# Kernel optimization log

Hardware: AMD Instinct MI355X
Metric: run time of the kernel (lower is better)

The kernel has to match this reference:

```python
import jax, jax.numpy as jnp
import numpy as np

B, N, S, D = 32, 128, 64, 512
MAX_LEN = 5000


def make_pe(d_model, max_len):
    pos = np.arange(max_len, dtype=np.float32)[:, None]
    div = np.exp(np.arange(0, d_model, 2, dtype=np.float32) * (-np.log(10000.0) / d_model))
    pe = np.zeros((max_len, d_model), dtype=np.float32)
    pe[:, 0::2] = np.sin(pos * div)
    pe[:, 1::2] = np.cos(pos * div)
    return jnp.asarray(pe)


def setup_inputs() -> dict:
    key = jax.random.key(0)
    ks = jax.random.split(key, 16)
    s1 = 1.0 / np.sqrt(D)
    s2 = 1.0 / np.sqrt(2 * D)
    inp = {
        "x": jax.random.normal(ks[0], (B, N), jnp.float32),
        "timesteps": jax.random.randint(ks[1], (B,), 0, 1000),
        "fusion_feat": jax.random.normal(ks[2], (B, D), jnp.float32),
        "tar_image_feat": jax.random.normal(ks[3], (B, N, S, D), jnp.float32),
        "pe": make_pe(D, MAX_LEN),
        # torch Linear weights are [out, in]
        "Wq": jax.random.normal(ks[4], (D, D), jnp.float32) * s1,
        "Wk": jax.random.normal(ks[5], (D, D), jnp.float32) * s1,
        "Wv": jax.random.normal(ks[6], (D, D), jnp.float32) * s1,
        "Wp": jax.random.normal(ks[7], (D, D), jnp.float32) * s1,
        "bp": jnp.zeros((D,), jnp.float32),
        "Wt1": jax.random.normal(ks[8], (D, D), jnp.float32) * s1,
        "bt1": jnp.zeros((D,), jnp.float32),
        "Wt2": jax.random.normal(ks[9], (D, D), jnp.float32) * s1,
        "bt2": jnp.zeros((D,), jnp.float32),
        "Wd1": jax.random.normal(ks[10], (2 * D, 2 * D), jnp.float32) * s2,
        "bd1": jnp.zeros((2 * D,), jnp.float32),
        "Wd2": jax.random.normal(ks[11], (1, 2 * D), jnp.float32) * s2,
        "bd2": jnp.zeros((1,), jnp.float32),
    }
    return inp


def reference(x, timesteps, fusion_feat, tar_image_feat, pe,
              Wq, Wk, Wv, Wp, bp, Wt1, bt1, Wt2, bt2, Wd1, bd1, Wd2, bd2):
    # timestep embedding: pe[timesteps] -> [B, D], then 2-layer SiLU MLP (eval mode: dropout off)
    cond = jax.nn.silu(pe[timesteps] @ Wt1.T + bt1) @ Wt2.T + bt2  # [B, D]

    # similarity argmax over S tokens, then gather best token per (b, n)
    sim = jnp.einsum('bd,bnsd->bns', fusion_feat, tar_image_feat)  # [B, N, S]
    best = jnp.argmax(sim, axis=-1)                                # [B, N]
    tif = jnp.take_along_axis(tar_image_feat, best[:, :, None, None], axis=2)[:, :, 0, :]  # [B, N, D]

    # single-vector attention over N candidates
    q = (fusion_feat + cond) @ Wq.T                  # [B, D]
    k = (tif + cond[:, None, :]) @ Wk.T              # [B, N, D]
    v = (tif + cond[:, None, :]) @ Wv.T              # [B, N, D]
    w = jax.nn.softmax(jnp.einsum('bd,bnd->bn', q, k) + x, axis=-1)  # [B, N]
    new_emb = jnp.einsum('bn,bnd->bd', w, v) @ Wp.T + bp             # [B, D]

    # MLP decode over concat [new_emb (broadcast), tif]
    emb = jnp.concatenate([jnp.broadcast_to(new_emb[:, None, :], tif.shape), tif], axis=-1)  # [B, N, 2D]
    h = jax.nn.relu(emb @ Wd1.T + bd1)
    p = (h @ Wd2.T + bd2)[..., 0] + w                # [B, N]

    # sort descending along N
    return -jnp.sort(-p, axis=1)
```

## Files before the change

### kernel.cpp

```cpp
#include <hip/hip_runtime.h>
#include <hip/hip_bf16.h>
#include <math.h>


#define BB 32
#define NN 128
#define SS 64
#define DD 512

typedef __attribute__((ext_vector_type(8))) short short8;
typedef __attribute__((ext_vector_type(4))) float f32x4;

__device__ __forceinline__ ushort f2bf(float f) {
    unsigned u = __float_as_uint(f);
    unsigned r = (u + 0x7fffu + ((u >> 16) & 1u)) >> 16;
    return (ushort)r;
}
__device__ __forceinline__ float bf2f(ushort u) {
    return __uint_as_float(((unsigned)u) << 16);
}

__device__ __forceinline__ void wave_dot512x4(
    const float* __restrict__ w, size_t ldw, float4 xa, float4 xb,
    int lane, float out[4]) {
    float4 ra[4], rb[4];
#pragma unroll
    for (int r = 0; r < 4; ++r) {
        const float4* row = reinterpret_cast<const float4*>(w + (size_t)r * ldw);
        ra[r] = row[lane * 2];
        rb[r] = row[lane * 2 + 1];
    }
#pragma unroll
    for (int r = 0; r < 4; ++r) {
        float s = ra[r].x * xa.x + ra[r].y * xa.y + ra[r].z * xa.z + ra[r].w * xa.w
                + rb[r].x * xb.x + rb[r].y * xb.y + rb[r].z * xb.z + rb[r].w * xb.w;
#pragma unroll
        for (int off = 32; off; off >>= 1) s += __shfl_xor(s, off);
        out[r] = s;
    }
}

__global__ __launch_bounds__(256) void bmv(
    const float* __restrict__ W, int ldw, const float* __restrict__ bias,
    const float* __restrict__ Xa, const float* __restrict__ Xb,
    const int* __restrict__ ts, const float* __restrict__ pe,
    float* __restrict__ Y, int R, int act, int mode) {
    __shared__ __align__(16) float xl[DD];
    int b = blockIdx.y, tid = threadIdx.x, lane = tid & 63, wave = tid >> 6;
    const float* src = (mode == 1) ? (pe + (size_t)ts[b] * DD) : (Xa + (size_t)b * DD);
    if (mode == 2) {
        const float* s2 = Xb + (size_t)b * DD;
        for (int i = tid; i < DD; i += 256) xl[i] = src[i] + s2[i];
    } else {
        for (int i = tid; i < DD; i += 256) xl[i] = src[i];
    }
    __syncthreads();
    float4 xa = reinterpret_cast<const float4*>(xl)[lane * 2];
    float4 xb = reinterpret_cast<const float4*>(xl)[lane * 2 + 1];
    int j0 = blockIdx.x * 16 + wave * 4;
    float s[4];
    wave_dot512x4(W + (size_t)j0 * ldw, ldw, xa, xb, lane, s);
    if (lane < 4) {
        int j = j0 + lane;
        float v = s[lane];
        if (bias) v += bias[j];
        if (act == 1) v = v / (1.f + expf(-v));
        Y[(size_t)b * R + j] = v;
    }
}

__global__ __launch_bounds__(256) void k_qk(
    const float* __restrict__ Wk, const float* __restrict__ q,
    float* __restrict__ qk) {
    __shared__ __align__(16) float ql[DD];
    __shared__ float part[4][64];
    int b = blockIdx.y, c0 = blockIdx.x * 64;
    int tid = threadIdx.x, lane = tid & 63, wave = tid >> 6;
    for (int i = tid; i < DD; i += 256) ql[i] = q[(size_t)b * DD + i];
    __syncthreads();
    float p = 0.f;
    for (int j = wave * 128; j < wave * 128 + 128; ++j)
        p += ql[j] * Wk[(size_t)j * DD + c0 + lane];
    part[wave][lane] = p;
    __syncthreads();
    if (tid < 64)
        qk[(size_t)b * DD + c0 + tid] =
            part[0][tid] + part[1][tid] + part[2][tid] + part[3][tid];
}

__global__ __launch_bounds__(256) void k2_sim(
    const float* __restrict__ fusion, const float* __restrict__ tif,
    const float* __restrict__ x, const float* __restrict__ qk,
    const float* __restrict__ Wd1, ushort* __restrict__ Wb,
    ushort* __restrict__ abf, float* __restrict__ score) {
    __shared__ __align__(16) float fb[DD];
    __shared__ float bv_s[4];
    __shared__ int bi_s[4];
    __shared__ int bidx_s;
    __shared__ float dred[4];
    int bn = blockIdx.x, b = bn >> 7;
    int tid = threadIdx.x, lane = tid & 63, wave = tid >> 6;

    if (bn < 1024) {
        int idx = (bn * 256 + tid) * 2;
        int r = idx >> 9, k = idx & 511;
        float2 v = *reinterpret_cast<const float2*>(Wd1 + (size_t)r * 1024 + 512 + k);
        ushort2 o = {f2bf(v.x), f2bf(v.y)};
        *reinterpret_cast<ushort2*>(Wb + (size_t)r * 512 + k) = o;
    }

    for (int i = tid; i < DD; i += 256) fb[i] = fusion[(size_t)b * DD + i];
    __syncthreads();
    float4 xa = reinterpret_cast<const float4*>(fb)[lane * 2];
    float4 xb = reinterpret_cast<const float4*>(fb)[lane * 2 + 1];
    const float* base = tif + (size_t)bn * SS * DD;
    float bv = -INFINITY;
    int bi = 0;
    for (int s0 = wave * 16; s0 < wave * 16 + 16; s0 += 4) {
        float sv[4];
        wave_dot512x4(base + (size_t)s0 * DD, DD, xa, xb, lane, sv);
#pragma unroll
        for (int r = 0; r < 4; ++r)
            if (sv[r] > bv) { bv = sv[r]; bi = s0 + r; }
    }
    if (lane == 0) { bv_s[wave] = bv; bi_s[wave] = bi; }
    __syncthreads();
    if (tid == 0) {
        float v = bv_s[0]; int i0 = bi_s[0];
        for (int w = 1; w < 4; w++)
            if (bv_s[w] > v) { v = bv_s[w]; i0 = bi_s[w]; }
        bidx_s = i0;
    }
    __syncthreads();
    const float* src = base + (size_t)bidx_s * DD;
    const float* qkb = qk + (size_t)b * DD;
    float local = 0.f;
    for (int i = tid; i < DD; i += 256) {
        float vv = src[i];
        abf[(size_t)bn * DD + i] = f2bf(vv);
        local += vv * qkb[i];
    }
#pragma unroll
    for (int off = 32; off; off >>= 1) local += __shfl_xor(local, off);
    if (lane == 0) dred[wave] = local;
    __syncthreads();
    if (tid == 0) score[bn] = dred[0] + dred[1] + dred[2] + dred[3] + x[bn];
}

__global__ __launch_bounds__(256) void k_vsum(
    const float* __restrict__ score, const ushort* __restrict__ abf,
    const float* __restrict__ cond,
    float* __restrict__ wout, float* __restrict__ vsum) {
    __shared__ float wl[NN];
    __shared__ float redm[2], reds[2];
    int b = blockIdx.y, tid = threadIdx.x, lane = tid & 63, wave = tid >> 6;
    float v = 0.f;
    if (tid < NN) {
        v = score[b * NN + tid];
        float m = v;
#pragma unroll
        for (int off = 32; off; off >>= 1) m = fmaxf(m, __shfl_xor(m, off));
        if (lane == 0) redm[wave] = m;
    }
    __syncthreads();
    float m = fmaxf(redm[0], redm[1]);
    if (tid < NN) {
        float e = expf(v - m);
        wl[tid] = e;
        float s = e;
#pragma unroll
        for (int off = 32; off; off >>= 1) s += __shfl_xor(s, off);
        if (lane == 0) reds[wave] = s;
    }
    __syncthreads();
    float inv = 1.f / (reds[0] + reds[1]);
    if (blockIdx.x == 0 && tid < NN) wout[b * NN + tid] = wl[tid] * inv;
    int d = blockIdx.x * 256 + tid;
    const ushort* base = abf + (size_t)b * NN * DD + d;
    float s = 0.f;
#pragma unroll 8
    for (int n = 0; n < NN; n++) s += wl[n] * bf2f(base[(size_t)n * DD]);
    vsum[(size_t)b * DD + d] = s * inv + cond[(size_t)b * DD + d];
}

__global__ __launch_bounds__(256) void k4_mfma(
    const ushort* __restrict__ Abf, const ushort* __restrict__ Wb,
    const float* __restrict__ Wd1, const float* __restrict__ bd1,
    const float* __restrict__ ne, const float* __restrict__ Wd2,
    float* __restrict__ p_part) {
    __shared__ ushort aS[2][128 * 64];
    __shared__ ushort bS[2][128 * 64];
    __shared__ __align__(16) float nel[DD];
    __shared__ float uloc[128];
    int tid = threadIdx.x, l = tid & 63, w = tid >> 6;
    int m0 = blockIdx.x * 128, n0 = blockIdx.y * 128;
    int b = blockIdx.x;
    int wm = w >> 1, wn = w & 1;

    for (int i = tid; i < DD; i += 256) nel[i] = ne[(size_t)b * DD + i];
    __syncthreads();
    float4 na = reinterpret_cast<const float4*>(nel)[l * 2];
    float4 nb = reinterpret_cast<const float4*>(nel)[l * 2 + 1];

#define STAGE(K0, BUF)                                                         \
    {                                                                          \
        _Pragma("unroll") for (int i = 0; i < 4; ++i) {                        \
            int L = i * 4096 + w * 1024 + l * 16;                              \
            int row = L >> 7;                                                  \
            int bo = L & 127;                                                  \
            int sb = bo ^ ((row & 7) << 4);                                    \
            const ushort* ga = Abf + (size_t)(m0 + row) * DD + (K0) + (sb >> 1); \
            const ushort* gb = Wb + (size_t)(n0 + row) * DD + (K0) + (sb >> 1);  \
            __builtin_amdgcn_global_load_lds(                                  \
                (const __attribute__((address_space(1))) void*)ga,             \
                (__attribute__((address_space(3))) void*)(aS[BUF] + i * 2048 + w * 512), \
                16, 0, 0);                                                     \
            __builtin_amdgcn_global_load_lds(                                  \
                (const __attribute__((address_space(1))) void*)gb,             \
                (__attribute__((address_space(3))) void*)(bS[BUF] + i * 2048 + w * 512), \
                16, 0, 0);                                                     \
        }                                                                      \
    }

    STAGE(0, 0);
    for (int j0 = 0; j0 < 32; j0 += 4) {
        int r = w * 32 + j0;
        float s[4];
        wave_dot512x4(Wd1 + (size_t)(n0 + r) * 1024, 1024, na, nb, l, s);
        if (l < 4) uloc[r + l] = s[l] + bd1[n0 + r + l];
    }
    __syncthreads();

    f32x4 acc[4][4];
#pragma unroll
    for (int i = 0; i < 4; i++)
#pragma unroll
        for (int j = 0; j < 4; j++) acc[i][j] = (f32x4){0.f, 0.f, 0.f, 0.f};

    int cur = 0;
    for (int k0 = 0; k0 < DD; k0 += 64) {
        if (k0 + 64 < DD) STAGE(k0 + 64, cur ^ 1);
#pragma unroll
        for (int kk = 0; kk < 2; ++kk) {
            short8 af[4], bf[4];
#pragma unroll
            for (int f = 0; f < 4; ++f) {
                int ra = wm * 64 + f * 16 + (l & 15);
                int boa = (((l >> 4) * 16 + kk * 64)) ^ ((ra & 7) << 4);
                af[f] = *reinterpret_cast<const short8*>(&aS[cur][ra * 64 + (boa >> 1)]);
                int rb = wn * 64 + f * 16 + (l & 15);
                int bob = (((l >> 4) * 16 + kk * 64)) ^ ((rb & 7) << 4);
                bf[f] = *reinterpret_cast<const short8*>(&bS[cur][rb * 64 + (bob >> 1)]);
            }
#pragma unroll
            for (int fm = 0; fm < 4; ++fm)
#pragma unroll
                for (int fn = 0; fn < 4; ++fn)
                    acc[fm][fn] = __builtin_amdgcn_mfma_f32_16x16x32_bf16(
                        af[fm], bf[fn], acc[fm][fn], 0, 0, 0);
        }
        __syncthreads();
        cur ^= 1;
    }
#undef STAGE
#pragma unroll
    for (int fm = 0; fm < 4; ++fm) {
#pragma unroll
        for (int reg = 0; reg < 4; ++reg) {
            float pp = 0.f;
#pragma unroll
            for (int fn = 0; fn < 4; ++fn) {
                int rl = wn * 64 + fn * 16 + (l & 15);
                float hh = acc[fm][fn][reg] + uloc[rl];
                if (hh > 0.f) pp += Wd2[n0 + rl] * hh;
            }
#pragma unroll
            for (int off = 1; off < 16; off <<= 1) pp += __shfl_xor(pp, off);
            if ((l & 15) == 0) {
                int m = m0 + wm * 64 + fm * 16 + (l >> 4) * 4 + reg;
                p_part[(size_t)m * 16 + blockIdx.y * 2 + wn] = pp;
            }
        }
    }
}

__global__ __launch_bounds__(128) void k5_sort(
    const float* __restrict__ p_part, const float* __restrict__ wout,
    const float* __restrict__ bd2, float* __restrict__ out) {
    __shared__ float v[NN];
    int b = blockIdx.x, tid = threadIdx.x;
    int bn = b * NN + tid;
    float s = bd2[0] + wout[bn];
#pragma unroll
    for (int c = 0; c < 16; c++) s += p_part[(size_t)bn * 16 + c];
    v[tid] = s;
    __syncthreads();
    for (int k = 2; k <= NN; k <<= 1) {
        for (int j = k >> 1; j > 0; j >>= 1) {
            int ixj = tid ^ j;
            if (ixj > tid) {
                float a = v[tid], bb2 = v[ixj];
                bool desc = (tid & k) == 0;
                if (desc ? (a < bb2) : (a > bb2)) { v[tid] = bb2; v[ixj] = a; }
            }
            __syncthreads();
        }
    }
    out[bn] = v[tid];
}

extern "C" void kernel_launch(void* const* d_in, const int* in_sizes, int n_in,
                              void* d_out, int out_size, void* d_ws, size_t ws_size,
                              hipStream_t stream) {
    const float* x      = (const float*)d_in[0];
    const int*   ts     = (const int*)d_in[1];
    const float* fusion = (const float*)d_in[2];
    const float* tif    = (const float*)d_in[3];
    const float* pe     = (const float*)d_in[4];
    const float* Wq     = (const float*)d_in[5];
    const float* Wk     = (const float*)d_in[6];
    const float* Wv     = (const float*)d_in[7];
    const float* Wp     = (const float*)d_in[8];
    const float* bp     = (const float*)d_in[9];
    const float* Wt1    = (const float*)d_in[10];
    const float* bt1    = (const float*)d_in[11];
    const float* Wt2    = (const float*)d_in[12];
    const float* bt2    = (const float*)d_in[13];
    const float* Wd1    = (const float*)d_in[14];
    const float* bd1    = (const float*)d_in[15];
    const float* Wd2    = (const float*)d_in[16];
    const float* bd2    = (const float*)d_in[17];

    float* ws = (float*)d_ws;
    float* cond     = ws;
    float* qk       = cond + 16384;
    float* h        = qk + 16384;
    float* q        = h + 16384;
    float* score    = q + 16384;
    float* wout     = score + 4096;
    float* vsum     = wout + 4096;
    float* ve       = vsum + 16384;
    float* ne       = ve + 16384;
    float* p_part   = ne + 16384;
    ushort* Abf     = (ushort*)(p_part + 65536);
    ushort* Wb      = Abf + 2097152;
    float* out = (float*)d_out;

    hipLaunchKernelGGL(bmv, dim3(32, BB), dim3(256), 0, stream,
                       Wt1, DD, bt1, nullptr, nullptr, ts, pe, h, DD, 1, 1);
    hipLaunchKernelGGL(bmv, dim3(32, BB), dim3(256), 0, stream,
                       Wt2, DD, bt2, h, nullptr, nullptr, nullptr, cond, DD, 0, 0);
    hipLaunchKernelGGL(bmv, dim3(32, BB), dim3(256), 0, stream,
                       Wq, DD, nullptr, fusion, cond, nullptr, nullptr, q, DD, 0, 2);
    hipLaunchKernelGGL(k_qk, dim3(8, BB), dim3(256), 0, stream, Wk, q, qk);

    hipLaunchKernelGGL(k2_sim, dim3(BB * NN), dim3(256), 0, stream,
                       fusion, tif, x, qk, Wd1, Wb, Abf, score);

    hipLaunchKernelGGL(k_vsum, dim3(2, BB), dim3(256), 0, stream,
                       score, Abf, cond, wout, vsum);
    hipLaunchKernelGGL(bmv, dim3(32, BB), dim3(256), 0, stream,
                       Wv, DD, nullptr, vsum, nullptr, nullptr, nullptr, ve, DD, 0, 0);
    hipLaunchKernelGGL(bmv, dim3(32, BB), dim3(256), 0, stream,
                       Wp, DD, bp, ve, nullptr, nullptr, nullptr, ne, DD, 0, 0);

    hipLaunchKernelGGL(k4_mfma, dim3(32, 8), dim3(256), 0, stream,
                       Abf, Wb, Wd1, bd1, ne, Wd2, p_part);
    hipLaunchKernelGGL(k5_sort, dim3(BB), dim3(128), 0, stream,
                       p_part, wout, bd2, out);
}
```

Measured before the change: 181.9 us.

## Fold Wp·Wv and Wkᵀ·Wq into precomputed matrices to cut matvec stages

Adds a kernel that computes Wp·Wv and Wkᵀ·Wq with an fp32 tiled GEMM each call. q·Wk is then obtained in one batched matvec using the combined matrix, and the value and projection matvecs collapse into one. This removes two launches and the intermediate q and ve buffers. In exchange it adds two 512×512×512 matrix products per call, which may cost more than the small matvecs saved.

```diff
diff --git a/kernel.cpp b/kernel.cpp
--- a/kernel.cpp
+++ b/kernel.cpp
@@ -37,6 +37,97 @@
 #pragma unroll
         for (int off = 32; off; off >>= 1) s += __shfl_xor(s, off);
         out[r] = s;
+    }
+}
+
+__global__ __launch_bounds__(256) void k_wprep(
+    const float* __restrict__ Wp, const float* __restrict__ Wv,
+    const float* __restrict__ Wk, const float* __restrict__ Wq,
+    float* __restrict__ Wpv, float* __restrict__ Mk) {
+    __shared__ __align__(16) float buf[32 * 68 + 32 * 64];
+    int g = blockIdx.x, tid = threadIdx.x;
+    int t0 = (tid & 15) * 4, t1 = (tid >> 4) * 4;
+    float acc[4][4] = {};
+    if (g < 64) {
+        int i0 = (g & 7) * 64, d0 = (g >> 3) * 64;
+        float* wp_t = buf;
+        float* wv_s = buf + 32 * 68;
+        for (int j0 = 0; j0 < DD; j0 += 32) {
+#pragma unroll
+            for (int q2 = 0; q2 < 2; ++q2) {
+                int s = tid * 2 + q2;
+                int i = s >> 3, j4 = (s & 7) * 4;
+                float4 v = *reinterpret_cast<const float4*>(
+                    Wp + (size_t)(i0 + i) * DD + j0 + j4);
+                wp_t[(j4 + 0) * 68 + i] = v.x; wp_t[(j4 + 1) * 68 + i] = v.y;
+                wp_t[(j4 + 2) * 68 + i] = v.z; wp_t[(j4 + 3) * 68 + i] = v.w;
+            }
+#pragma unroll
+            for (int q2 = 0; q2 < 2; ++q2) {
+                int s = tid * 2 + q2;
+                int j = s >> 4, d4 = (s & 15) * 4;
+                *reinterpret_cast<float4*>(&wv_s[j * 64 + d4]) =
+                    *reinterpret_cast<const float4*>(
+                        Wv + (size_t)(j0 + j) * DD + d0 + d4);
+            }
+            __syncthreads();
+#pragma unroll 8
+            for (int j = 0; j < 32; ++j) {
+                float4 a = *reinterpret_cast<const float4*>(&wp_t[j * 68 + t0]);
+                float4 bv = *reinterpret_cast<const float4*>(&wv_s[j * 64 + t1]);
+                float a_[4] = {a.x, a.y, a.z, a.w};
+                float b_[4] = {bv.x, bv.y, bv.z, bv.w};
+#pragma unroll
+                for (int e = 0; e < 4; ++e)
+#pragma unroll
+                    for (int f = 0; f < 4; ++f) acc[e][f] += a_[e] * b_[f];
+            }
+            __syncthreads();
+        }
+#pragma unroll
+        for (int e = 0; e < 4; ++e)
+            *reinterpret_cast<float4*>(&Wpv[(size_t)(i0 + t0 + e) * DD + d0 + t1]) =
+                *reinterpret_cast<float4*>(acc[e]);
+    } else {
+        int g2 = g - 64;
+        int c0 = (g2 & 7) * 64, i0 = (g2 >> 3) * 64;
+        float* wk_s = buf;
+        float* wq_s = buf + 32 * 68;
+        for (int j0 = 0; j0 < DD; j0 += 32) {
+#pragma unroll
+            for (int q2 = 0; q2 < 2; ++q2) {
+                int s = tid * 2 + q2;
+                int j = s >> 4, c4 = (s & 15) * 4;
+                float4 v = *reinterpret_cast<const float4*>(
+                    Wk + (size_t)(j0 + j) * DD + c0 + c4);
+                *reinterpret_cast<float4*>(&wk_s[j * 68 + c4]) = v;
+            }
+#pragma unroll
+            for (int q2 = 0; q2 < 2; ++q2) {
+                int s = tid * 2 + q2;
+                int j = s >> 4, i4 = (s & 15) * 4;
+                *reinterpret_cast<float4*>(&wq_s[j * 64 + i4]) =
+                    *reinterpret_cast<const float4*>(
+                        Wq + (size_t)(j0 + j) * DD + i0 + i4);
+            }
+            __syncthreads();
+#pragma unroll 8
+            for (int j = 0; j < 32; ++j) {
+                float4 a = *reinterpret_cast<const float4*>(&wk_s[j * 68 + t0]);
+                float4 bv = *reinterpret_cast<const float4*>(&wq_s[j * 64 + t1]);
+                float a_[4] = {a.x, a.y, a.z, a.w};
+                float b_[4] = {bv.x, bv.y, bv.z, bv.w};
+#pragma unroll
+                for (int e = 0; e < 4; ++e)
+#pragma unroll
+                    for (int f = 0; f < 4; ++f) acc[e][f] += a_[e] * b_[f];
+            }
+            __syncthreads();
+        }
+#pragma unroll
+        for (int e = 0; e < 4; ++e)
+            *reinterpret_cast<float4*>(&Mk[(size_t)(c0 + t0 + e) * DD + i0 + t1]) =
+                *reinterpret_cast<float4*>(acc[e]);
     }
 }
 
@@ -67,25 +158,6 @@
         if (act == 1) v = v / (1.f + expf(-v));
         Y[(size_t)b * R + j] = v;
     }
-}
-
-__global__ __launch_bounds__(256) void k_qk(
-    const float* __restrict__ Wk, const float* __restrict__ q,
-    float* __restrict__ qk) {
-    __shared__ __align__(16) float ql[DD];
-    __shared__ float part[4][64];
-    int b = blockIdx.y, c0 = blockIdx.x * 64;
-    int tid = threadIdx.x, lane = tid & 63, wave = tid >> 6;
-    for (int i = tid; i < DD; i += 256) ql[i] = q[(size_t)b * DD + i];
-    __syncthreads();
-    float p = 0.f;
-    for (int j = wave * 128; j < wave * 128 + 128; ++j)
-        p += ql[j] * Wk[(size_t)j * DD + c0 + lane];
-    part[wave][lane] = p;
-    __syncthreads();
-    if (tid < 64)
-        qk[(size_t)b * DD + c0 + tid] =
-            part[0][tid] + part[1][tid] + part[2][tid] + part[3][tid];
 }
 
 __global__ __launch_bounds__(256) void k2_sim(
@@ -335,24 +407,26 @@
     float* cond     = ws;
     float* qk       = cond + 16384;
     float* h        = qk + 16384;
-    float* q        = h + 16384;
-    float* score    = q + 16384;
+    float* score    = h + 16384;
     float* wout     = score + 4096;
     float* vsum     = wout + 4096;
-    float* ve       = vsum + 16384;
-    float* ne       = ve + 16384;
-    float* p_part   = ne + 16384;
+    float* ne       = vsum + 16384;
+    float* Mk       = ne + 16384;
+    float* Wpv      = Mk + 262144;
+    float* p_part   = Wpv + 262144;
     ushort* Abf     = (ushort*)(p_part + 65536);
     ushort* Wb      = Abf + 2097152;
     float* out = (float*)d_out;
+
+    hipLaunchKernelGGL(k_wprep, dim3(128), dim3(256), 0, stream,
+                       Wp, Wv, Wk, Wq, Wpv, Mk);
 
     hipLaunchKernelGGL(bmv, dim3(32, BB), dim3(256), 0, stream,
                        Wt1, DD, bt1, nullptr, nullptr, ts, pe, h, DD, 1, 1);
     hipLaunchKernelGGL(bmv, dim3(32, BB), dim3(256), 0, stream,
                        Wt2, DD, bt2, h, nullptr, nullptr, nullptr, cond, DD, 0, 0);
     hipLaunchKernelGGL(bmv, dim3(32, BB), dim3(256), 0, stream,
-                       Wq, DD, nullptr, fusion, cond, nullptr, nullptr, q, DD, 0, 2);
-    hipLaunchKernelGGL(k_qk, dim3(8, BB), dim3(256), 0, stream, Wk, q, qk);
+                       Mk, DD, nullptr, fusion, cond, nullptr, nullptr, qk, DD, 0, 2);
 
     hipLaunchKernelGGL(k2_sim, dim3(BB * NN), dim3(256), 0, stream,
                        fusion, tif, x, qk, Wd1, Wb, Abf, score);
@@ -360,9 +434,7 @@
     hipLaunchKernelGGL(k_vsum, dim3(2, BB), dim3(256), 0, stream,
                        score, Abf, cond, wout, vsum);
     hipLaunchKernelGGL(bmv, dim3(32, BB), dim3(256), 0, stream,
-                       Wv, DD, nullptr, vsum, nullptr, nullptr, nullptr, ve, DD, 0, 0);
-    hipLaunchKernelGGL(bmv, dim3(32, BB), dim3(256), 0, stream,
-                       Wp, DD, bp, ve, nullptr, nullptr, nullptr, ne, DD, 0, 0);
+                       Wpv, DD, bp, vsum, nullptr, nullptr, nullptr, ne, DD, 0, 0);
 
     hipLaunchKernelGGL(k4_mfma, dim3(32, 8), dim3(256), 0, stream,
                        Abf, Wb, Wd1, bd1, ne, Wd2, p_part);
```

Result: slower. 199.6 us (+9.7%).
